# Optimization experiments

Hardware: AMD Instinct MI355X
Metric: run time of the kernel (lower is better)

The kernel has to match this reference:

```python
import jax, jax.numpy as jnp
from jax import lax
import numpy as np

DIM = 512
NUM_HEADS = 8
SR = 2


def setup_inputs() -> dict:
    key = jax.random.key(0)
    ks = jax.random.split(key, 7)
    B, H, W = 4, 64, 64
    N = H * W
    C = DIM
    s = 0.02
    return {
        "x": jax.random.normal(ks[0], (B, N, C), dtype=jnp.float32),
        "q_w": jax.random.normal(ks[1], (C, C), dtype=jnp.float32) * s,
        "kv_w": jax.random.normal(ks[2], (2 * C, C), dtype=jnp.float32) * s,
        "sr_w": jax.random.normal(ks[3], (C, C, SR, SR), dtype=jnp.float32) * s,
        "sr_b": jax.random.normal(ks[4], (C,), dtype=jnp.float32) * s,
        "proj_w": jax.random.normal(ks[5], (C, C), dtype=jnp.float32) * s,
        "proj_b": jax.random.normal(ks[6], (C,), dtype=jnp.float32) * s,
        "H": H,
        "W": W,
    }


def reference(x, q_w, kv_w, sr_w, sr_b, proj_w, proj_b, H, W):
    B, N, C = x.shape
    nh = NUM_HEADS
    hd = C // nh
    scale = hd ** -0.5

    # q projection: [B, nh, N, hd]
    q = (x @ q_w.T).reshape(B, N, nh, hd).transpose(0, 2, 1, 3)

    # spatial reduction via strided conv (kernel=stride=SR)
    x_ = x.transpose(0, 2, 1).reshape(B, C, H, W)
    x_ = lax.conv_general_dilated(
        x_, sr_w, window_strides=(SR, SR), padding="VALID",
        dimension_numbers=("NCHW", "OIHW", "NCHW"),
    ) + sr_b[None, :, None, None]
    Nk = (H // SR) * (W // SR)
    x_ = x_.reshape(B, C, Nk).transpose(0, 2, 1)  # [B, Nk, C]

    # kv projection: [2, B, nh, Nk, hd]
    kv = (x_ @ kv_w.T).reshape(B, Nk, 2, nh, hd).transpose(2, 0, 3, 1, 4)
    k, v = kv[0], kv[1]

    attn = jax.nn.softmax(jnp.einsum("bhnd,bhmd->bhnm", q, k) * scale, axis=-1)
    out = jnp.einsum("bhnm,bhmd->bhnd", attn, v)  # [B, nh, N, hd]
    out = out.transpose(0, 2, 1, 3).reshape(B, N, C)
    return out @ proj_w.T + proj_b
```

## Files before the change

kernel.cpp:

```cpp
#include <hip/hip_runtime.h>


typedef __attribute__((ext_vector_type(8)))  short short8;
typedef __attribute__((ext_vector_type(8)))  unsigned short ushort8;
typedef __attribute__((ext_vector_type(4)))  float floatx4;
typedef __attribute__((ext_vector_type(16))) float floatx16;

__device__ inline unsigned short bf16r(float f) {
    union { float f; unsigned u; } v; v.f = f;
    unsigned r = v.u + 0x7fffu + ((v.u >> 16) & 1u);
    return (unsigned short)(r >> 16);
}

__device__ inline ushort8 pack8(float4 a, float4 b) {
    ushort8 o;
    o[0] = bf16r(a.x); o[1] = bf16r(a.y); o[2] = bf16r(a.z); o[3] = bf16r(a.w);
    o[4] = bf16r(b.x); o[5] = bf16r(b.y); o[6] = bf16r(b.z); o[7] = bf16r(b.w);
    return o;
}

__device__ inline void gl_lds16(const void* g, void* l) {
    __builtin_amdgcn_global_load_lds(
        (const __attribute__((address_space(1))) unsigned int*)g,
        (__attribute__((address_space(3))) unsigned int*)l, 16, 0, 0);
}

__global__ __launch_bounds__(256)
void convert_all(const float* __restrict__ x,  const float* __restrict__ qw,
                 const float* __restrict__ kvw, const float* __restrict__ srw,
                 const float* __restrict__ pw,
                 unsigned short* __restrict__ xb,  unsigned short* __restrict__ qwb,
                 unsigned short* __restrict__ kvwb, unsigned short* __restrict__ srwb,
                 unsigned short* __restrict__ pwb) {
    const int bid = blockIdx.x;
    const float* src; unsigned short* dst; int off; float sc = 1.f;
    if (bid < 4096)      { src = x;   dst = xb;   off = bid * 256; }
    else if (bid < 4224) { src = qw;  dst = qwb;  off = (bid - 4096) * 256;
                           sc = 0.18033688011112042f;  }
    else if (bid < 4480) { src = kvw; dst = kvwb; off = (bid - 4224) * 256; }
    else if (bid < 4992) { src = srw; dst = srwb; off = (bid - 4480) * 256; }
    else                 { src = pw;  dst = pwb;  off = (bid - 4992) * 256; }
    const int idx = off + threadIdx.x;
    float4 a = *(const float4*)(src + (size_t)idx * 8);
    float4 b = *(const float4*)(src + (size_t)idx * 8 + 4);
    a.x *= sc; a.y *= sc; a.z *= sc; a.w *= sc;
    b.x *= sc; b.y *= sc; b.z *= sc; b.w *= sc;
    *(ushort8*)(dst + (size_t)idx * 8) = pack8(a, b);
}

__global__ __launch_bounds__(256)
void gather_xr_f32(const float* __restrict__ x, unsigned short* __restrict__ xrb) {
    const int idx = blockIdx.x * 256 + threadIdx.x;
    const int c = idx & 511;
    const int m = idx >> 9;
    const int b = m >> 10;
    const int rem = m & 1023;
    const int oi = rem >> 5, oj = rem & 31;
    const int n00 = oi * 128 + oj * 2;
    const float* base = x + ((size_t)b * 4096) * 512 + c;
    const unsigned long long v00 = bf16r(base[(size_t)(n00)      * 512]);
    const unsigned long long v01 = bf16r(base[(size_t)(n00 + 1)  * 512]);
    const unsigned long long v10 = bf16r(base[(size_t)(n00 + 64) * 512]);
    const unsigned long long v11 = bf16r(base[(size_t)(n00 + 65) * 512]);
    const unsigned long long w = v00 | (v01 << 16) | (v10 << 32) | (v11 << 48);
    *(unsigned long long*)(xrb + (size_t)m * 2048 + c * 4) = w;
}

template<int BM, int MODE>
__global__ __launch_bounds__(256)
void gemm_mfma(const unsigned short* __restrict__ A,
               const unsigned short* __restrict__ B,
               const float* __restrict__ bias,
               float* __restrict__ Cf, unsigned short* __restrict__ Cb,
               int M, int N, int K) {
    constexpr int MI = BM / 32;
    __shared__ unsigned short As[BM * 32];
    __shared__ unsigned short Bs[128 * 32];
    const int t = threadIdx.x;
    const int w = t >> 6, l = t & 63;
    const int lq = l & 15, quad = l >> 4;
    const int bm = blockIdx.x * BM, bn = blockIdx.y * 128;
    const int wrow = (w >> 1) * (BM / 2), wcol = (w & 1) * 64;

    floatx4 acc[MI][4];
    #pragma unroll
    for (int mi = 0; mi < MI; ++mi)
        #pragma unroll
        for (int ni = 0; ni < 4; ++ni) acc[mi][ni] = (floatx4){0.f, 0.f, 0.f, 0.f};

    for (int k0 = 0; k0 < K; k0 += 32) {
        __syncthreads();
        #pragma unroll
        for (int i = 0; i < BM / 64; ++i) {
            const int c = i * 256 + t;
            gl_lds16(A + (size_t)(bm + (c >> 2)) * K + k0 + (c & 3) * 8, &As[c * 8]);
        }
        #pragma unroll
        for (int i = 0; i < 2; ++i) {
            const int c = i * 256 + t;
            gl_lds16(B + (size_t)(bn + (c >> 2)) * K + k0 + (c & 3) * 8, &Bs[c * 8]);
        }
        __syncthreads();

        short8 bf[4];
        #pragma unroll
        for (int ni = 0; ni < 4; ++ni)
            bf[ni] = *(const short8*)&Bs[(wcol + ni * 16 + lq) * 32 + quad * 8];
        #pragma unroll
        for (int mi = 0; mi < MI; ++mi) {
            const short8 af = *(const short8*)&As[(wrow + mi * 16 + lq) * 32 + quad * 8];
            #pragma unroll
            for (int ni = 0; ni < 4; ++ni)
                acc[mi][ni] = __builtin_amdgcn_mfma_f32_16x16x32_bf16(
                    af, bf[ni], acc[mi][ni], 0, 0, 0);
        }
    }

    #pragma unroll
    for (int ni = 0; ni < 4; ++ni) {
        const int col = bn + wcol + ni * 16 + lq;
        const float bv = (MODE <= 1 && bias) ? bias[col] : 0.f;
        #pragma unroll
        for (int mi = 0; mi < MI; ++mi) {
            const int row0 = bm + wrow + mi * 16 + quad * 4;
            if (MODE == 0) {
                #pragma unroll
                for (int r = 0; r < 4; ++r)
                    Cf[(size_t)(row0 + r) * N + col] = acc[mi][ni][r] + bv;
            } else if (MODE == 1) {
                unsigned own[4], mg[4];
                #pragma unroll
                for (int r = 0; r < 4; ++r) own[r] = bf16r(acc[mi][ni][r] + bv);
                #pragma unroll
                for (int r = 0; r < 4; ++r) {
                    const unsigned pt = __shfl_xor(own[r], 1);
                    mg[r] = (lq & 1) ? (pt | (own[r] << 16)) : (own[r] | (pt << 16));
                }
                const int colb = bn + wcol + ni * 16 + (lq & ~1);
                const int rb = (lq & 1) * 2;
                *(unsigned*)(Cb + (size_t)(row0 + rb)     * N + colb) = mg[rb];
                *(unsigned*)(Cb + (size_t)(row0 + rb + 1) * N + colb) = mg[rb + 1];
            } else if (MODE == 2) {
                const int kb = col >> 10, key = col & 1023;
                const int h = row0 >> 6, d0 = row0 & 63;
                unsigned long long wv = 0;
                #pragma unroll
                for (int r = 0; r < 4; ++r)
                    wv |= (unsigned long long)bf16r(acc[mi][ni][r]) << (16 * r);
                *(unsigned long long*)(Cb +
                    (((size_t)(kb * 8 + h)) * 1024 + key) * 64 + d0) = wv;
            } else {
                const int kb = row0 >> 10, key0 = row0 & 1023;
                const int h = col >> 6, d = col & 63;
                unsigned long long wv = 0;
                #pragma unroll
                for (int r = 0; r < 4; ++r)
                    wv |= (unsigned long long)bf16r(acc[mi][ni][r]) << (16 * r);
                *(unsigned long long*)(Cb +
                    (((size_t)(kb * 8 + h)) * 64 + d) * 1024 + key0) = wv;
            }
        }
    }
}

#define KS2 72

__global__ __launch_bounds__(256)
void attn_mfma32(const unsigned short* __restrict__ qb,
                 const unsigned short* __restrict__ Kb,
                 const unsigned short* __restrict__ Vt,
                 unsigned short* __restrict__ out) {
    __shared__ unsigned short Ks[64 * KS2];
    __shared__ unsigned short Vs[64 * KS2];

    const int t = threadIdx.x;
    const int w = t >> 6;
    const int lane = t & 63;
    const int m32 = lane & 31;
    const int sig = lane >> 5;
    const int n0 = blockIdx.x * 128;
    const int bh = blockIdx.y;
    const int b = bh >> 3, h = bh & 7;

    short8 qf[4];
    {
        const unsigned short* qrow =
            qb + ((size_t)(b * 4096 + n0 + w * 32 + m32)) * 512 + h * 64;
        #pragma unroll
        for (int kc = 0; kc < 4; ++kc)
            qf[kc] = *(const short8*)(qrow + kc * 16 + sig * 8);
    }

    float l_own = 0.f;
    floatx16 O0, O1;
    #pragma unroll
    for (int i = 0; i < 16; ++i) { O0[i] = 0.f; O1[i] = 0.f; }

    const unsigned short* Kg = Kb + (size_t)bh * 1024 * 64;
    const unsigned short* Vg = Vt + (size_t)bh * 64 * 1024;
    const int srow = t >> 2;
    const int sdb  = (t & 3) * 16;

    for (int kt = 0; kt < 16; ++kt) {
        __syncthreads();
        {
            const unsigned short* src = Kg + ((size_t)(kt * 64 + srow)) * 64 + sdb;
            *(ushort8*)&Ks[srow * KS2 + sdb]     = *(const ushort8*)src;
            *(ushort8*)&Ks[srow * KS2 + sdb + 8] = *(const ushort8*)(src + 8);
        }
        {
            const unsigned short* src = Vg + (size_t)srow * 1024 + kt * 64 + sdb;
            *(ushort8*)&Vs[srow * KS2 + sdb]     = *(const ushort8*)src;
            *(ushort8*)&Vs[srow * KS2 + sdb + 8] = *(const ushort8*)(src + 8);
        }
        __syncthreads();

        floatx16 st0, st1;
        #pragma unroll
        for (int i = 0; i < 16; ++i) { st0[i] = 0.f; st1[i] = 0.f; }
        #pragma unroll
        for (int kc = 0; kc < 4; ++kc) {
            const short8 a0 = *(const short8*)&Ks[m32 * KS2 + kc * 16 + sig * 8];
            st0 = __builtin_amdgcn_mfma_f32_32x32x16_bf16(a0, qf[kc], st0, 0, 0, 0);
            const short8 a1 = *(const short8*)&Ks[(32 + m32) * KS2 + kc * 16 + sig * 8];
            st1 = __builtin_amdgcn_mfma_f32_32x32x16_bf16(a1, qf[kc], st1, 0, 0, 0);
        }

        uint2 E[2][4];
        #pragma unroll
        for (int g = 0; g < 2; ++g) {
            #pragma unroll
            for (int qd = 0; qd < 4; ++qd) {
                const float s0 = g ? st1[qd * 4 + 0] : st0[qd * 4 + 0];
                const float s1 = g ? st1[qd * 4 + 1] : st0[qd * 4 + 1];
                const float s2 = g ? st1[qd * 4 + 2] : st0[qd * 4 + 2];
                const float s3 = g ? st1[qd * 4 + 3] : st0[qd * 4 + 3];
                const unsigned u0 = __float_as_uint(__builtin_amdgcn_exp2f(s0));
                const unsigned u1 = __float_as_uint(__builtin_amdgcn_exp2f(s1));
                const unsigned u2 = __float_as_uint(__builtin_amdgcn_exp2f(s2));
                const unsigned u3 = __float_as_uint(__builtin_amdgcn_exp2f(s3));
                E[g][qd].x = __builtin_amdgcn_perm(u1, u0, 0x07060302u);
                E[g][qd].y = __builtin_amdgcn_perm(u3, u2, 0x07060302u);
                l_own += __uint_as_float(u0 & 0xffff0000u)
                       + __uint_as_float(u1 & 0xffff0000u)
                       + __uint_as_float(u2 & 0xffff0000u)
                       + __uint_as_float(u3 & 0xffff0000u);
            }
        }

        #pragma unroll
        for (int kc = 0; kc < 4; ++kc) {
            const int g = kc >> 1, qlo = (kc & 1) * 2;
            const uint2 keep = sig ? E[g][qlo + 1] : E[g][qlo];
            const uint2 send = sig ? E[g][qlo]     : E[g][qlo + 1];
            uint2 got;
            got.x = __shfl_xor(send.x, 32);
            got.y = __shfl_xor(send.y, 32);
            uint4 fr;
            fr.x = sig ? got.x  : keep.x;
            fr.y = sig ? got.y  : keep.y;
            fr.z = sig ? keep.x : got.x;
            fr.w = sig ? keep.y : got.y;
            const short8 pa = *(const short8*)&fr;
            const short8 v0 = *(const short8*)&Vs[m32 * KS2 + kc * 16 + sig * 8];
            O0 = __builtin_amdgcn_mfma_f32_32x32x16_bf16(pa, v0, O0, 0, 0, 0);
            const short8 v1 = *(const short8*)&Vs[(32 + m32) * KS2 + kc * 16 + sig * 8];
            O1 = __builtin_amdgcn_mfma_f32_32x32x16_bf16(pa, v1, O1, 0, 0, 0);
        }
    }

    l_own += __shfl_xor(l_own, 32);
    const float inv = 1.0f / l_own;

    float fo0[16], fo1[16];
    #pragma unroll
    for (int r = 0; r < 16; ++r) {
        const float li = __shfl(inv, ((r & 3) + 8 * (r >> 2)) + 4 * sig);
        fo0[r] = O0[r] * li;
        fo1[r] = O1[r] * li;
    }

    #pragma unroll
    for (int gd = 0; gd < 2; ++gd) {
        unsigned mg[16];
        #pragma unroll
        for (int r = 0; r < 16; ++r) {
            const unsigned own = bf16r(gd ? fo1[r] : fo0[r]);
            const unsigned pt = __shfl_xor(own, 1);
            mg[r] = (m32 & 1) ? (pt | (own << 16)) : (own | (pt << 16));
        }
        if ((m32 & 1) == gd) {
            const int colb = h * 64 + gd * 32 + (m32 & ~1);
            #pragma unroll
            for (int r = 0; r < 16; ++r) {
                const int qrow = (r & 3) + 8 * (r >> 2) + 4 * sig;
                const size_t row = (size_t)(b * 4096 + n0 + w * 32 + qrow);
                *(unsigned*)(out + row * 512 + colb) = mg[r];
            }
        }
    }
}

extern "C" void kernel_launch(void* const* d_in, const int* in_sizes, int n_in,
                              void* d_out, int out_size, void* d_ws, size_t ws_size,
                              hipStream_t stream) {
    const float* x      = (const float*)d_in[0];
    const float* q_w    = (const float*)d_in[1];
    const float* kv_w   = (const float*)d_in[2];
    const float* sr_w   = (const float*)d_in[3];
    const float* sr_b   = (const float*)d_in[4];
    const float* proj_w = (const float*)d_in[5];
    const float* proj_b = (const float*)d_in[6];
    float* out = (float*)d_out;

    unsigned short* xb   = (unsigned short*)d_ws;
    unsigned short* attb = xb;
    unsigned short* qb   = xb   + (size_t)16384 * 512;
    unsigned short* xrb  = qb   + (size_t)16384 * 512;
    unsigned short* xsrb = xrb  + (size_t)4096 * 2048;
    unsigned short* qwb  = xsrb + (size_t)4096 * 512;
    unsigned short* kvwb = qwb  + (size_t)512 * 512;
    unsigned short* srwb = kvwb + (size_t)1024 * 512;
    unsigned short* pwb  = srwb + (size_t)512 * 2048;
    unsigned short* Kb   = pwb  + (size_t)512 * 512;
    unsigned short* Vt   = Kb   + (size_t)32 * 1024 * 64;

    const dim3 blk(256);

    convert_all<<<5120, blk, 0, stream>>>(x, q_w, kv_w, sr_w, proj_w,
                                          xb, qwb, kvwb, srwb, pwb);

    gather_xr_f32<<<8192, blk, 0, stream>>>(x, xrb);

    gemm_mfma<128, 1><<<dim3(128, 4), blk, 0, stream>>>(
        xb, qwb, nullptr, nullptr, qb, 16384, 512, 512);

    gemm_mfma<64, 1><<<dim3(64, 4), blk, 0, stream>>>(
        xrb, srwb, sr_b, nullptr, xsrb, 4096, 512, 2048);

    gemm_mfma<128, 2><<<dim3(4, 32), blk, 0, stream>>>(
        kvwb, xsrb, nullptr, nullptr, Kb, 512, 4096, 512);

    gemm_mfma<128, 3><<<dim3(32, 4), blk, 0, stream>>>(
        xsrb, kvwb + (size_t)512 * 512, nullptr, nullptr, Vt, 4096, 512, 512);

    attn_mfma32<<<dim3(32, 32), blk, 0, stream>>>(qb, Kb, Vt, attb);

    gemm_mfma<128, 0><<<dim3(128, 4), blk, 0, stream>>>(
        attb, pwb, proj_b, out, nullptr, 16384, 512, 512);
}
```

Baseline: 260.6 us.

## Merge prep kernels, add BN=64 GEMM tiles, simplify softmax row-sum

```diff
diff --git a/kernel.cpp b/kernel.cpp
--- a/kernel.cpp
+++ b/kernel.cpp
@@ -26,61 +26,62 @@
 }
 
 __global__ __launch_bounds__(256)
-void convert_all(const float* __restrict__ x,  const float* __restrict__ qw,
-                 const float* __restrict__ kvw, const float* __restrict__ srw,
-                 const float* __restrict__ pw,
-                 unsigned short* __restrict__ xb,  unsigned short* __restrict__ qwb,
-                 unsigned short* __restrict__ kvwb, unsigned short* __restrict__ srwb,
-                 unsigned short* __restrict__ pwb) {
+void prep(const float* __restrict__ x,  const float* __restrict__ qw,
+          const float* __restrict__ kvw, const float* __restrict__ srw,
+          const float* __restrict__ pw,
+          unsigned short* __restrict__ xb,  unsigned short* __restrict__ qwb,
+          unsigned short* __restrict__ kvwb, unsigned short* __restrict__ srwb,
+          unsigned short* __restrict__ pwb, unsigned short* __restrict__ xrb) {
     const int bid = blockIdx.x;
-    const float* src; unsigned short* dst; int off; float sc = 1.f;
-    if (bid < 4096)      { src = x;   dst = xb;   off = bid * 256; }
-    else if (bid < 4224) { src = qw;  dst = qwb;  off = (bid - 4096) * 256;
-                           sc = 0.18033688011112042f;  }
-    else if (bid < 4480) { src = kvw; dst = kvwb; off = (bid - 4224) * 256; }
-    else if (bid < 4992) { src = srw; dst = srwb; off = (bid - 4480) * 256; }
-    else                 { src = pw;  dst = pwb;  off = (bid - 4992) * 256; }
-    const int idx = off + threadIdx.x;
-    float4 a = *(const float4*)(src + (size_t)idx * 8);
-    float4 b = *(const float4*)(src + (size_t)idx * 8 + 4);
-    a.x *= sc; a.y *= sc; a.z *= sc; a.w *= sc;
-    b.x *= sc; b.y *= sc; b.z *= sc; b.w *= sc;
-    *(ushort8*)(dst + (size_t)idx * 8) = pack8(a, b);
-}
-
-__global__ __launch_bounds__(256)
-void gather_xr_f32(const float* __restrict__ x, unsigned short* __restrict__ xrb) {
-    const int idx = blockIdx.x * 256 + threadIdx.x;
-    const int c = idx & 511;
-    const int m = idx >> 9;
-    const int b = m >> 10;
-    const int rem = m & 1023;
-    const int oi = rem >> 5, oj = rem & 31;
-    const int n00 = oi * 128 + oj * 2;
-    const float* base = x + ((size_t)b * 4096) * 512 + c;
-    const unsigned long long v00 = bf16r(base[(size_t)(n00)      * 512]);
-    const unsigned long long v01 = bf16r(base[(size_t)(n00 + 1)  * 512]);
-    const unsigned long long v10 = bf16r(base[(size_t)(n00 + 64) * 512]);
-    const unsigned long long v11 = bf16r(base[(size_t)(n00 + 65) * 512]);
-    const unsigned long long w = v00 | (v01 << 16) | (v10 << 32) | (v11 << 48);
-    *(unsigned long long*)(xrb + (size_t)m * 2048 + c * 4) = w;
-}
-
-template<int BM, int MODE>
+    if (bid < 5120) {
+        const float* src; unsigned short* dst; int off; float sc = 1.f;
+        if (bid < 4096)      { src = x;   dst = xb;   off = bid * 256; }
+        else if (bid < 4224) { src = qw;  dst = qwb;  off = (bid - 4096) * 256;
+                               sc = 0.18033688011112042f;  }
+        else if (bid < 4480) { src = kvw; dst = kvwb; off = (bid - 4224) * 256; }
+        else if (bid < 4992) { src = srw; dst = srwb; off = (bid - 4480) * 256; }
+        else                 { src = pw;  dst = pwb;  off = (bid - 4992) * 256; }
+        const int idx = off + threadIdx.x;
+        float4 a = *(const float4*)(src + (size_t)idx * 8);
+        float4 b = *(const float4*)(src + (size_t)idx * 8 + 4);
+        a.x *= sc; a.y *= sc; a.z *= sc; a.w *= sc;
+        b.x *= sc; b.y *= sc; b.z *= sc; b.w *= sc;
+        *(ushort8*)(dst + (size_t)idx * 8) = pack8(a, b);
+    } else {
+        const int idx = (bid - 5120) * 256 + threadIdx.x;
+        const int c = idx & 511;
+        const int m = idx >> 9;
+        const int b = m >> 10;
+        const int rem = m & 1023;
+        const int oi = rem >> 5, oj = rem & 31;
+        const int n00 = oi * 128 + oj * 2;
+        const float* base = x + ((size_t)b * 4096) * 512 + c;
+        const unsigned long long v00 = bf16r(base[(size_t)(n00)      * 512]);
+        const unsigned long long v01 = bf16r(base[(size_t)(n00 + 1)  * 512]);
+        const unsigned long long v10 = bf16r(base[(size_t)(n00 + 64) * 512]);
+        const unsigned long long v11 = bf16r(base[(size_t)(n00 + 65) * 512]);
+        const unsigned long long w = v00 | (v01 << 16) | (v10 << 32) | (v11 << 48);
+        *(unsigned long long*)(xrb + (size_t)m * 2048 + c * 4) = w;
+    }
+}
+
+template<int BM, int BN, int MODE>
 __global__ __launch_bounds__(256)
 void gemm_mfma(const unsigned short* __restrict__ A,
                const unsigned short* __restrict__ B,
                const float* __restrict__ bias,
                float* __restrict__ Cf, unsigned short* __restrict__ Cb,
                int M, int N, int K) {
-    constexpr int MI = BM / 32;
+    constexpr int WR = (BN == 128) ? BM / 2 : BM / 4;
+    constexpr int MI = WR / 16;
     __shared__ unsigned short As[BM * 32];
-    __shared__ unsigned short Bs[128 * 32];
+    __shared__ unsigned short Bs[BN * 32];
     const int t = threadIdx.x;
     const int w = t >> 6, l = t & 63;
     const int lq = l & 15, quad = l >> 4;
-    const int bm = blockIdx.x * BM, bn = blockIdx.y * 128;
-    const int wrow = (w >> 1) * (BM / 2), wcol = (w & 1) * 64;
+    const int bm = blockIdx.x * BM, bn = blockIdx.y * BN;
+    const int wrow = (BN == 128) ? (w >> 1) * (BM / 2) : w * (BM / 4);
+    const int wcol = (BN == 128) ? (w & 1) * 64 : 0;
 
     floatx4 acc[MI][4];
     #pragma unroll
@@ -96,7 +97,7 @@
             gl_lds16(A + (size_t)(bm + (c >> 2)) * K + k0 + (c & 3) * 8, &As[c * 8]);
         }
         #pragma unroll
-        for (int i = 0; i < 2; ++i) {
+        for (int i = 0; i < BN / 64; ++i) {
             const int c = i * 256 + t;
             gl_lds16(B + (size_t)(bn + (c >> 2)) * K + k0 + (c & 3) * 8, &Bs[c * 8]);
         }
@@ -231,20 +232,15 @@
         for (int g = 0; g < 2; ++g) {
             #pragma unroll
             for (int qd = 0; qd < 4; ++qd) {
-                const float s0 = g ? st1[qd * 4 + 0] : st0[qd * 4 + 0];
-                const float s1 = g ? st1[qd * 4 + 1] : st0[qd * 4 + 1];
-                const float s2 = g ? st1[qd * 4 + 2] : st0[qd * 4 + 2];
-                const float s3 = g ? st1[qd * 4 + 3] : st0[qd * 4 + 3];
-                const unsigned u0 = __float_as_uint(__builtin_amdgcn_exp2f(s0));
-                const unsigned u1 = __float_as_uint(__builtin_amdgcn_exp2f(s1));
-                const unsigned u2 = __float_as_uint(__builtin_amdgcn_exp2f(s2));
-                const unsigned u3 = __float_as_uint(__builtin_amdgcn_exp2f(s3));
-                E[g][qd].x = __builtin_amdgcn_perm(u1, u0, 0x07060302u);
-                E[g][qd].y = __builtin_amdgcn_perm(u3, u2, 0x07060302u);
-                l_own += __uint_as_float(u0 & 0xffff0000u)
-                       + __uint_as_float(u1 & 0xffff0000u)
-                       + __uint_as_float(u2 & 0xffff0000u)
-                       + __uint_as_float(u3 & 0xffff0000u);
+                const float p0 = __builtin_amdgcn_exp2f(g ? st1[qd * 4 + 0] : st0[qd * 4 + 0]);
+                const float p1 = __builtin_amdgcn_exp2f(g ? st1[qd * 4 + 1] : st0[qd * 4 + 1]);
+                const float p2 = __builtin_amdgcn_exp2f(g ? st1[qd * 4 + 2] : st0[qd * 4 + 2]);
+                const float p3 = __builtin_amdgcn_exp2f(g ? st1[qd * 4 + 3] : st0[qd * 4 + 3]);
+                E[g][qd].x = __builtin_amdgcn_perm(
+                    __float_as_uint(p1), __float_as_uint(p0), 0x07060302u);
+                E[g][qd].y = __builtin_amdgcn_perm(
+                    __float_as_uint(p3), __float_as_uint(p2), 0x07060302u);
+                l_own += (p0 + p1) + (p2 + p3);
             }
         }
 
@@ -327,25 +323,23 @@
 
     const dim3 blk(256);
 
-    convert_all<<<5120, blk, 0, stream>>>(x, q_w, kv_w, sr_w, proj_w,
-                                          xb, qwb, kvwb, srwb, pwb);
-
-    gather_xr_f32<<<8192, blk, 0, stream>>>(x, xrb);
-
-    gemm_mfma<128, 1><<<dim3(128, 4), blk, 0, stream>>>(
+    prep<<<13312, blk, 0, stream>>>(x, q_w, kv_w, sr_w, proj_w,
+                                    xb, qwb, kvwb, srwb, pwb, xrb);
+
+    gemm_mfma<128, 64, 1><<<dim3(128, 8), blk, 0, stream>>>(
         xb, qwb, nullptr, nullptr, qb, 16384, 512, 512);
 
-    gemm_mfma<64, 1><<<dim3(64, 4), blk, 0, stream>>>(
+    gemm_mfma<64, 64, 1><<<dim3(64, 8), blk, 0, stream>>>(
         xrb, srwb, sr_b, nullptr, xsrb, 4096, 512, 2048);
 
-    gemm_mfma<128, 2><<<dim3(4, 32), blk, 0, stream>>>(
+    gemm_mfma<128, 64, 2><<<dim3(4, 64), blk, 0, stream>>>(
         kvwb, xsrb, nullptr, nullptr, Kb, 512, 4096, 512);
 
-    gemm_mfma<128, 3><<<dim3(32, 4), blk, 0, stream>>>(
+    gemm_mfma<128, 64, 3><<<dim3(32, 8), blk, 0, stream>>>(
         xsrb, kvwb + (size_t)512 * 512, nullptr, nullptr, Vt, 4096, 512, 512);
 
     attn_mfma32<<<dim3(32, 32), blk, 0, stream>>>(qb, Kb, Vt, attb);
 
-    gemm_mfma<128, 0><<<dim3(128, 4), blk, 0, stream>>>(
+    gemm_mfma<128, 64, 0><<<dim3(128, 8), blk, 0, stream>>>(
         attb, pwb, proj_b, out, nullptr, 16384, 512, 512);
 }
```

Result: faster. 245.1 us (-5.9%).
